# Kernel optimization log

Hardware: AMD Instinct MI355X
Metric: run time of the kernel (lower is better)

## Reference

```python
import jax, jax.numpy as jnp
import numpy as np
from itertools import product

# Static geometry (matches init_kwargs)
Z, H, W = 8, 96, 180
WZ, WH, WW = 2, 6, 12
MZ, MH, MW = Z // WZ, H // WH, W // WW   # 4, 16, 15
WP = WZ * WH * WW                        # 144 tokens per window
WN = MZ * MH * MW                        # 960 windows
DIM, HEADS = 384, 12
DH = DIM // HEADS
SHIFT = (WZ // 2, WH // 2, WW // 2)      # (1, 3, 6)
NBIAS = WZ * WZ * WH * WH * (2 * WW - 1) # 3312 bias entries
WT = MZ * MH                             # 64 window types (vary with Z,H only)


def _position_index():
    zi = np.arange(WZ); zj = -np.arange(WZ) * WZ
    hi = np.arange(WH); hj = -np.arange(WH) * WH
    w = np.arange(WW)
    c1 = np.stack(np.meshgrid(zi, hi, w, indexing='ij')).reshape(3, WP, 1)
    c2 = np.stack(np.meshgrid(zj, hj, w, indexing='ij')).reshape(3, 1, WP)
    coords = (c1 - c2).transpose(1, 2, 0).astype(np.int64)  # (WP, WP, 3)
    coords[:, :, 2] += WW - 1
    coords[:, :, 1] *= 2 * WW - 1
    coords[:, :, 0] *= (2 * WW - 1) * WH * WH
    return coords.sum(-1).reshape(-1)  # (WP*WP,)


def _attention_mask():
    # in_shape divisible by window -> pad mask is all-zero; only shifted-window
    # (non-adjacency) mask remains, exactly as in the torch buffer.
    img = np.ones((Z, H, W), np.float32)
    zs = (slice(0, -WZ), slice(-WZ, -SHIFT[0]), slice(-SHIFT[0], None))
    hs = (slice(0, -WH), slice(-WH, -SHIFT[1]), slice(-SHIFT[1], None))
    ws = (slice(0, -WW), slice(-WW, -SHIFT[2]), slice(-SHIFT[2], None))
    cnt = 0
    for z, h, w in product(zs, hs, ws):
        img[z, h, w] = cnt
        cnt += 1
    mw = img.reshape(MZ, WZ, MH, WH, MW, WW).transpose(0, 2, 4, 1, 3, 5).reshape(WN, WP)
    diff = mw[:, None, :] - mw[:, :, None]
    return np.where(diff != 0, -100.0, 0.0).astype(np.float32)


POS_IDX = jnp.asarray(_position_index())
ATTN_MASK = jnp.asarray(_attention_mask())  # (WN, WP, WP)


def _layernorm(x, w, b, eps=1e-5):
    m = jnp.mean(x, axis=-1, keepdims=True)
    v = jnp.mean(jnp.square(x - m), axis=-1, keepdims=True)
    return (x - m) * jax.lax.rsqrt(v + eps) * w + b


def setup_inputs() -> dict:
    key = jax.random.key(0)
    ks = jax.random.split(key, 8)
    s = 0.02
    return {
        'x': jax.random.normal(ks[0], (1, Z * H * W, DIM), jnp.float32),
        'w_qkv': jax.random.normal(ks[1], (DIM, 3 * DIM), jnp.float32) * s,
        'w_proj': jax.random.normal(ks[2], (DIM, DIM), jnp.float32) * s,
        'b_proj': jnp.zeros((DIM,), jnp.float32),
        'bias_table': jax.random.normal(ks[3], (NBIAS, WT, HEADS), jnp.float32) * 0.02,
        'ln1_w': jnp.ones((DIM,), jnp.float32),
        'ln1_b': jnp.zeros((DIM,), jnp.float32),
        'ln2_w': jnp.ones((DIM,), jnp.float32),
        'ln2_b': jnp.zeros((DIM,), jnp.float32),
        'w1': jax.random.normal(ks[4], (DIM, 4 * DIM), jnp.float32) * s,
        'b1': jnp.zeros((4 * DIM,), jnp.float32),
        'w2': jax.random.normal(ks[5], (4 * DIM, DIM), jnp.float32) * s,
        'b2': jnp.zeros((DIM,), jnp.float32),
    }


def reference(x, w_qkv, w_proj, b_proj, bias_table, ln1_w, ln1_b, ln2_w, ln2_b, w1, b1, w2, b2):
    B = x.shape[0]
    shortcut = x
    # (B, Z*H*W, D) -> (B, Z, H, W, D); pad is identity (divisible shapes)
    xg = x.reshape(B, Z, H, W, DIM)
    xg = jnp.roll(xg, (-SHIFT[0], -SHIFT[1], -SHIFT[2]), axis=(1, 2, 3))
    # window partition -> (B*WN, WP, D) with window order (B, mZ, mH, mW)
    xw = xg.reshape(B, MZ, WZ, MH, WH, MW, WW, DIM)
    xw = xw.transpose(0, 1, 3, 5, 2, 4, 6, 7).reshape(B * WN, WP, DIM)

    # ---- EarthAttention3D ----
    qkv = (xw @ w_qkv).reshape(B * WN, WP, 3, HEADS, DH).transpose(2, 0, 3, 1, 4)
    q = qkv[0] * (DH ** -0.5)
    k, v = qkv[1], qkv[2]
    attn = jnp.einsum('bhid,bhjd->bhij', q, k)  # (B*WN, HEADS, WP, WP)

    # earth-specific bias: one bias per (mZ, mH) window type, shared over B, mW
    bias = bias_table[POS_IDX].reshape(WP, WP, WT, HEADS).transpose(2, 3, 0, 1)
    bias = bias.reshape(MZ, MH, HEADS, WP, WP)
    attn = attn.reshape(B, MZ, MH, MW, HEADS, WP, WP) + bias[None, :, :, None]

    # shifted-window mask
    attn = attn.reshape(B, WN, HEADS, WP, WP) + ATTN_MASK[None, :, None]
    attn = jax.nn.softmax(attn, axis=-1).reshape(B * WN, HEADS, WP, WP)

    out = jnp.einsum('bhij,bhjd->bhid', attn, v)
    out = out.transpose(0, 2, 1, 3).reshape(B * WN, WP, DIM)
    out = out @ w_proj + b_proj

    # ---- window reverse, unroll, crop (identity) ----
    xg = out.reshape(B, MZ, MH, MW, WZ, WH, WW, DIM)
    xg = xg.transpose(0, 1, 4, 2, 5, 3, 6, 7).reshape(B, Z, H, W, DIM)
    xg = jnp.roll(xg, SHIFT, axis=(1, 2, 3))
    attn_out = xg.reshape(B, Z * H * W, DIM)

    # Pangu post-norm residuals (drop_path prob = 0 -> identity)
    x = shortcut + _layernorm(attn_out, ln1_w, ln1_b)
    h = jax.nn.gelu(x @ w1 + b1, approximate=False) @ w2 + b2
    x = x + _layernorm(h, ln2_w, ln2_b)
    return x
```

## Files before the change

### kernel.cpp

```cpp
#include <hip/hip_runtime.h>
#include <hip/hip_bf16.h>
#include <math.h>

typedef __hip_bfloat16 bf16;
typedef __attribute__((ext_vector_type(4))) float f32x4;
typedef __attribute__((ext_vector_type(16))) float f32x16;
typedef __attribute__((ext_vector_type(8))) short s16x8;
typedef __attribute__((ext_vector_type(4))) short s16x4;

#define DEVI __device__ __forceinline__

constexpr int ZD = 8, HD = 96, WD = 180;
constexpr int WZ = 2, WH = 6, WWn = 12;
constexpr int MZ = 4, MH = 16, MW = 15;
constexpr int WP = 144, WN = 960;
constexpr int DIM = 384, HEADS = 12, DH = 32;
constexpr int TOK = ZD * HD * WD;
constexpr size_t TOKDIM = (size_t)TOK * DIM;
constexpr int NC = 3, CM = TOK / NC;

DEVI short f2b(float f) {
    bf16 h = __float2bfloat16(f);
    return *reinterpret_cast<short*>(&h);
}

DEVI int row_to_token(int r) {
    int wn = r / WP;
    int p  = r - wn * WP;
    int mz = wn / (MH * MW);
    int rem = wn - mz * (MH * MW);
    int mh = rem / MW;
    int mw = rem - mh * MW;
    int lz = p / (WH * WWn);
    int rp = p - lz * (WH * WWn);
    int lh = rp / WWn;
    int lw = rp - lh * WWn;
    int zp = mz * WZ + lz + 1;  if (zp >= ZD) zp -= ZD;
    int hp = mh * WH + lh + 3;  if (hp >= HD) hp -= HD;
    int wp = mw * WWn + lw + 6; if (wp >= WD) wp -= WD;
    return (zp * HD + hp) * WD + wp;
}


__global__ __launch_bounds__(256)
void k_fill(float* __restrict__ out, int n, float v) {
    int i = blockIdx.x * blockDim.x + threadIdx.x;
    if (i < n) out[i] = v;
}

__global__ __launch_bounds__(256)
void k_wcast(const float* __restrict__ w, bf16* __restrict__ wt, int K, int N) {
    int idx = blockIdx.x * blockDim.x + threadIdx.x;
    if (idx >= K * N) return;
    int n = idx / K;
    int k = idx - n * K;
    wt[idx] = __float2bfloat16(w[(size_t)k * N + n]);
}

__global__ __launch_bounds__(256)
void k_btr(const float* __restrict__ bt, float* __restrict__ btr) {
    int idx = blockIdx.x * blockDim.x + threadIdx.x;
    if (idx >= 64 * 12 * 3312) return;
    int wth = idx / 3312;
    int pos = idx - wth * 3312;
    btr[idx] = bt[(size_t)pos * 768 + wth] * 1.4426950408889634f;
}

__global__ __launch_bounds__(256)
void k_mktab(const float* __restrict__ btr, bf16* __restrict__ tab) {
    int idx = blockIdx.x * blockDim.x + threadIdx.x;
    if (idx >= 768 * WP * WP) return;
    int t = idx / (WP * WP);
    int e = idx - t * (WP * WP);
    int i = e / WP, j = e - i * WP;
    int wt = t / 12;
    int mz = wt >> 4, mh = wt & 15;
    int lzi = i / 72, ri_ = i - lzi * 72, lhi = ri_ / 12, lwi = ri_ - lhi * 12;
    int lzj = j / 72, rj_ = j - lzj * 72, lhj = rj_ / 12, lwj = rj_ - lhj * 12;
    int cA = lzi * 828 + lhi * 23 + lwi;
    int cB = lzj * 1656 + lhj * 138 + (11 - lwj);
    float vv = btr[(size_t)t * 3312 + cA + cB];
    int zri = (mz == 3) ? (lzi + 1) : 0, zrj = (mz == 3) ? (lzj + 1) : 0;
    int hri = (mh == 15) ? (lhi < 3 ? 1 : 2) : 0, hrj = (mh == 15) ? (lhj < 3 ? 1 : 2) : 0;
    if (zri != zrj || hri != hrj) vv -= 144.26950408889634f;
    tab[idx] = __float2bfloat16(vv);
}

__global__ __launch_bounds__(256)
void k_gather_x(const float* __restrict__ x, bf16* __restrict__ xw) {
    int idx = blockIdx.x * blockDim.x + threadIdx.x;
    if (idx >= TOK * 96) return;
    int r  = idx / 96;
    int c4 = (idx - r * 96) * 4;
    int t  = row_to_token(r);
    const float4 vv = *(const float4*)(x + (size_t)t * DIM + c4);
    s16x4 o;
    o[0] = f2b(vv.x); o[1] = f2b(vv.y); o[2] = f2b(vv.z); o[3] = f2b(vv.w);
    *(s16x4*)((short*)xw + (size_t)r * DIM + c4) = o;
}


DEVI void gload16(const bf16* g, bf16* l) {
    __builtin_amdgcn_global_load_lds(
        (const __attribute__((address_space(1))) void*)g,
        (__attribute__((address_space(3))) void*)l, 16, 0, 0);
}

template <int EPI>
__global__ __launch_bounds__(256)
void k_gemm(const bf16* __restrict__ A, const bf16* __restrict__ BT,
            const float* __restrict__ bias, bf16* __restrict__ out,
            int M, int N, int K) {
    constexpr int BK = 64;
    __shared__ bf16 As[128 * BK];
    __shared__ bf16 Bs[128 * BK];

    const int nb = N >> 7;
    const int g = blockIdx.x;
    const int xcd = g & 7;
    const int ii = g >> 3;
    const int tt = ii / nb;
    const int bm = tt * 8 + xcd;
    const int bn = ii - tt * nb;

    const int tid = threadIdx.x;
    const int lane = tid & 63;
    const int wv = tid >> 6;
    const int wr = wv >> 1;
    const int wc = wv & 1;
    const int l31 = lane & 31, hi = lane >> 5;

    const bf16* Ab = A + (size_t)bm * 128 * K;
    const bf16* Bb = BT + (size_t)bn * 128 * K;

    f32x16 acc[2][2] = {{{}, {}}, {{}, {}}};

    const int kiters = K / BK;
    const int srow = lane >> 3;
    const int scol = ((lane & 7) ^ srow) * 8;

    int ra[2], rb[2], rax[2], rbx[2];
#pragma unroll
    for (int i2 = 0; i2 < 2; i2++) {
        ra[i2] = 64 * wr + 32 * i2 + l31; rax[i2] = ra[i2] & 7;
        rb[i2] = 64 * wc + 32 * i2 + l31; rbx[i2] = rb[i2] & 7;
    }

    for (int kt = 0; kt < kiters; kt++) {
        const int k0 = kt * BK;
#pragma unroll
        for (int i = 0; i < 4; i++) {
            int ch = wv * 4 + i;
            int row = ch * 8 + srow;
            gload16(Ab + (size_t)row * K + k0 + scol, &As[ch * 512]);
            gload16(Bb + (size_t)row * K + k0 + scol, &Bs[ch * 512]);
        }
        asm volatile("s_waitcnt vmcnt(0)" ::: "memory");
        __syncthreads();
#pragma unroll
        for (int kk = 0; kk < 4; kk++) {
            const int s0 = 2 * kk + hi;
            s16x8 af[2], bfv[2];
#pragma unroll
            for (int ni = 0; ni < 2; ni++)
                af[ni] = *(const s16x8*)&Bs[ra[ni] * BK + ((s0 ^ rax[ni]) * 8)];
#pragma unroll
            for (int mi = 0; mi < 2; mi++)
                bfv[mi] = *(const s16x8*)&As[rb[mi] * BK + ((s0 ^ rbx[mi]) * 8)];
#pragma unroll
            for (int ni = 0; ni < 2; ni++)
#pragma unroll
                for (int mi = 0; mi < 2; mi++)
                    acc[ni][mi] = __builtin_amdgcn_mfma_f32_32x32x16_bf16(
                        af[ni], bfv[mi], acc[ni][mi], 0, 0, 0);
        }
        __syncthreads();
    }

    const int tokbase = bm * 128 + 64 * wc + l31;
    const int featbase = bn * 128 + 64 * wr + 4 * hi;
#pragma unroll
    for (int ni = 0; ni < 2; ni++) {
#pragma unroll
        for (int mi = 0; mi < 2; mi++) {
            const int tok = tokbase + 32 * mi;
#pragma unroll
            for (int rq = 0; rq < 4; rq++) {
                const int f0 = featbase + 32 * ni + 8 * rq;
                float v0 = acc[ni][mi][4 * rq + 0];
                float v1 = acc[ni][mi][4 * rq + 1];
                float v2 = acc[ni][mi][4 * rq + 2];
                float v3 = acc[ni][mi][4 * rq + 3];
                if constexpr (EPI == 0) {
                    const int which = f0 / DIM;
                    const int rem = f0 - which * DIM;
                    const int head = rem >> 5, dh = rem & 31;
                    if (which == 0) {
                        v0 *= 0.25503527f; v1 *= 0.25503527f;
                        v2 *= 0.25503527f; v3 *= 0.25503527f;
                    }
                    const int wn = tok / WP, p = tok - wn * WP;
                    s16x4 o; o[0] = f2b(v0); o[1] = f2b(v1); o[2] = f2b(v2); o[3] = f2b(v3);
                    *(s16x4*)(out + (size_t)which * TOKDIM +
                              ((size_t)(wn * HEADS + head) * WP + p) * DH + dh) = o;
                } else if constexpr (EPI == 1) {
                    const float4 bv = *(const float4*)(bias + f0);
                    s16x4 o;
                    o[0] = f2b(v0 + bv.x); o[1] = f2b(v1 + bv.y);
                    o[2] = f2b(v2 + bv.z); o[3] = f2b(v3 + bv.w);
                    *(s16x4*)(out + (size_t)tok * N + f0) = o;
                } else {
                    const float4 bv = *(const float4*)(bias + f0);
                    float g0 = v0 + bv.x, g1 = v1 + bv.y, g2 = v2 + bv.z, g3 = v3 + bv.w;
                    g0 = 0.5f * g0 * (1.0f + erff(g0 * 0.70710678118654752f));
                    g1 = 0.5f * g1 * (1.0f + erff(g1 * 0.70710678118654752f));
                    g2 = 0.5f * g2 * (1.0f + erff(g2 * 0.70710678118654752f));
                    g3 = 0.5f * g3 * (1.0f + erff(g3 * 0.70710678118654752f));
                    s16x4 o; o[0] = f2b(g0); o[1] = f2b(g1); o[2] = f2b(g2); o[3] = f2b(g3);
                    *(s16x4*)(out + (size_t)tok * N + f0) = o;
                }
            }
        }
    }
}

__global__ __launch_bounds__(192)
void k_attn(const bf16* __restrict__ q, const bf16* __restrict__ kmat,
            const bf16* __restrict__ v, const bf16* __restrict__ tab,
            bf16* __restrict__ out) {
    __shared__ bf16 Ks[WP * DH];
    __shared__ bf16 VTs[DH * 168];
    __shared__ bf16 Ps[3][16][168];
    __shared__ unsigned char regn[WP];

    const int bid = blockIdx.x;
    const int wn = bid / HEADS, head = bid - wn * HEADS;
    const int mz = wn / (MH * MW);
    const int rem = wn - mz * (MH * MW);
    const int mh = rem / MW, mw = rem - (rem / MW) * MW;
    const int tile = (mz * MH + mh) * HEADS + head;

    const int tid = threadIdx.x;
    const int lane = tid & 63;
    const int s = tid >> 6;
    const int lg = lane >> 4, lc = lane & 15;

    const size_t base = (size_t)(wn * HEADS + head) * (WP * DH);
    {
        short* vt = (short*)VTs;
#pragma unroll
        for (int e2 = 0; e2 < 3; e2++) {
            int idx = tid + 192 * e2;
            *(s16x8*)(Ks + idx * 8) = *(const s16x8*)(kmat + base + idx * 8);
            s16x8 vv = *(const s16x8*)(v + base + idx * 8);
            int p = idx >> 2;
            int d0 = (idx & 3) * 8;
#pragma unroll
            for (int e = 0; e < 8; e++) vt[(d0 + e) * 168 + p] = vv[e];
        }
        { int d = tid / 6, rm = tid - d * 6;
          *(s16x4*)(vt + d * 168 + 144 + rm * 4) = (s16x4){0, 0, 0, 0}; }
        { short* pz = (short*)&Ps[s][0][0];
          *(s16x4*)(pz + (lane >> 2) * 168 + 144 + (lane & 3) * 4) = (s16x4){0, 0, 0, 0}; }
        if (tid < WP) {
            int lz = tid / 72, rp = tid - lz * 72;
            int lh = rp / 12, lw = rp - lh * 12;
            int zr = (mz == 3) ? (lz + 1) : 0;
            int hr = (mh == 15) ? (lh < 3 ? 1 : 2) : 0;
            int wbit = (lw < 6) ? 1 : 2;
            regn[tid] = (unsigned char)((zr * 3 + hr) * 4 + wbit);
        }
    }
    __syncthreads();

    const f32x4 zf = {0.f, 0.f, 0.f, 0.f};
    const bf16* tb = tab + (size_t)tile * (WP * WP);
    bf16* ob = out + (size_t)wn * (WP * DIM) + head * DH;
    short* ps = (short*)&Ps[s][0][0];
    const bf16* psb = &Ps[s][0][0];

    for (int t = 0; t < 3; t++) {
        const int strip = 3 * s + t;
        const int ib = 16 * strip + 4 * lg;
        s16x8 aq = *(const s16x8*)(q + base + (size_t)(16 * strip + lc) * DH + 8 * lg);
        f32x4 sacc[9];
#pragma unroll
        for (int jt = 0; jt < 9; jt++) {
            s16x8 bk = *(const s16x8*)(Ks + (16 * jt + lc) * DH + 8 * lg);
            sacc[jt] = __builtin_amdgcn_mfma_f32_16x16x32_bf16(aq, bk, zf, 0, 0, 0);
        }
#pragma unroll
        for (int jt = 0; jt < 9; jt++) {
            int j = 16 * jt + lc;
#pragma unroll
            for (int r2 = 0; r2 < 4; r2++)
                sacc[jt][r2] += __bfloat162float(tb[(ib + r2) * WP + j]);
        }
        if (mw == 14) {
            int ri[4];
#pragma unroll
            for (int r2 = 0; r2 < 4; r2++) ri[r2] = regn[ib + r2];
#pragma unroll
            for (int jt = 0; jt < 9; jt++) {
                int rj = regn[16 * jt + lc];
#pragma unroll
                for (int r2 = 0; r2 < 4; r2++) {
                    bool m = ((ri[r2] >> 2) == (rj >> 2)) && ((ri[r2] & 3) != (rj & 3));
                    if (m) sacc[jt][r2] -= 144.2695f;
                }
            }
        }
        float inv[4];
#pragma unroll
        for (int r2 = 0; r2 < 4; r2++) {
            float sum = 0.f;
#pragma unroll
            for (int jt = 0; jt < 9; jt++) {
                float pe = exp2f(sacc[jt][r2]);
                sacc[jt][r2] = pe;
                sum += pe;
            }
#pragma unroll
            for (int o = 1; o < 16; o <<= 1) sum += __shfl_xor(sum, o);
            inv[r2] = 1.0f / sum;
        }
#pragma unroll
        for (int jt = 0; jt < 9; jt++)
#pragma unroll
            for (int r2 = 0; r2 < 4; r2++)
                ps[(4 * lg + r2) * 168 + 16 * jt + lc] = f2b(sacc[jt][r2]);
        f32x4 oacc[2] = {zf, zf};
#pragma unroll
        for (int c = 0; c < 5; c++) {
            s16x8 ap = *(const s16x8*)(psb + lc * 168 + 32 * c + 8 * lg);
#pragma unroll
            for (int nt = 0; nt < 2; nt++) {
                s16x8 bv = *(const s16x8*)(VTs + (16 * nt + lc) * 168 + 32 * c + 8 * lg);
                oacc[nt] = __builtin_amdgcn_mfma_f32_16x16x32_bf16(ap, bv, oacc[nt], 0, 0, 0);
            }
        }
#pragma unroll
        for (int nt = 0; nt < 2; nt++)
#pragma unroll
            for (int r2 = 0; r2 < 4; r2++)
                ob[(size_t)(ib + r2) * DIM + 16 * nt + lc] =
                    __float2bfloat16(oacc[nt][r2] * inv[r2]);
    }
}


__global__ __launch_bounds__(128)
void k_ln1(const bf16* __restrict__ y, const float* __restrict__ x,
           const float* __restrict__ w, const float* __restrict__ b,
           bf16* __restrict__ x1b, int r0) {
    __shared__ float red[4];
    const int rl = blockIdx.x, tid = threadIdx.x;
    const int t = row_to_token(r0 + rl);
    float v[3];
#pragma unroll
    for (int e = 0; e < 3; e++) v[e] = __bfloat162float(y[(size_t)rl * DIM + tid + 128 * e]);
    float s = v[0] + v[1] + v[2];
    float s2 = v[0] * v[0] + v[1] * v[1] + v[2] * v[2];
#pragma unroll
    for (int o = 1; o < 64; o <<= 1) { s += __shfl_xor(s, o); s2 += __shfl_xor(s2, o); }
    const int wv = tid >> 6;
    if ((tid & 63) == 0) { red[wv * 2] = s; red[wv * 2 + 1] = s2; }
    __syncthreads();
    s = red[0] + red[2]; s2 = red[1] + red[3];
    float mean = s * (1.f / 384.f);
    float var = fmaxf(s2 * (1.f / 384.f) - mean * mean, 0.f);
    float rs = rsqrtf(var + 1e-5f);
#pragma unroll
    for (int e = 0; e < 3; e++) {
        int c = tid + 128 * e;
        float o = (v[e] - mean) * rs * w[c] + b[c];
        float xo = x[(size_t)t * DIM + c] + o;
        ((short*)x1b)[(size_t)t * DIM + c] = f2b(xo);
    }
}

__global__ __launch_bounds__(128)
void k_ln2(const bf16* __restrict__ h, const bf16* __restrict__ x1b,
           const float* __restrict__ w, const float* __restrict__ b,
           float* __restrict__ out) {
    __shared__ float red[4];
    const int r = blockIdx.x, tid = threadIdx.x;
    float v[3];
#pragma unroll
    for (int e = 0; e < 3; e++) v[e] = __bfloat162float(h[(size_t)r * DIM + tid + 128 * e]);
    float s = v[0] + v[1] + v[2];
    float s2 = v[0] * v[0] + v[1] * v[1] + v[2] * v[2];
#pragma unroll
    for (int o = 1; o < 64; o <<= 1) { s += __shfl_xor(s, o); s2 += __shfl_xor(s2, o); }
    const int wv = tid >> 6;
    if ((tid & 63) == 0) { red[wv * 2] = s; red[wv * 2 + 1] = s2; }
    __syncthreads();
    s = red[0] + red[2]; s2 = red[1] + red[3];
    float mean = s * (1.f / 384.f);
    float var = fmaxf(s2 * (1.f / 384.f) - mean * mean, 0.f);
    float rs = rsqrtf(var + 1e-5f);
#pragma unroll
    for (int e = 0; e < 3; e++) {
        int c = tid + 128 * e;
        float o = (v[e] - mean) * rs * w[c] + b[c];
        out[(size_t)r * DIM + c] = __bfloat162float(x1b[(size_t)r * DIM + c]) + o;
    }
}


extern "C" void kernel_launch(void* const* d_in, const int* in_sizes, int n_in,
                              void* d_out, int out_size, void* d_ws, size_t ws_size,
                              hipStream_t stream) {
    const float* x      = (const float*)d_in[0];
    const float* w_qkv  = (const float*)d_in[1];
    const float* w_proj = (const float*)d_in[2];
    const float* b_proj = (const float*)d_in[3];
    const float* btab   = (const float*)d_in[4];
    const float* ln1w   = (const float*)d_in[5];
    const float* ln1b   = (const float*)d_in[6];
    const float* ln2w   = (const float*)d_in[7];
    const float* ln2b   = (const float*)d_in[8];
    const float* w1     = (const float*)d_in[9];
    const float* b1     = (const float*)d_in[10];
    const float* w2     = (const float*)d_in[11];
    const float* b2     = (const float*)d_in[12];

    const size_t NEED = 470237184ULL;
    if (ws_size < NEED) {
        k_fill<<<(out_size + 255) / 256, 256, 0, stream>>>((float*)d_out, out_size, 12345.0f);
        return;
    }

    char* ws = (char*)d_ws;
    bf16* wqkvT  = (bf16*)(ws + 0);
    bf16* wprojT = (bf16*)(ws + 884736);
    bf16* w1T    = (bf16*)(ws + 1179648);
    bf16* w2T    = (bf16*)(ws + 2359296);
    float* btr   = (float*)(ws + 3538944);
    bf16* tab    = (bf16*)(ws + 13713408);

    const size_t D1 = 45563904;
    const size_t D2 = 364068864;

    bf16* qkv  = (bf16*)(ws + D1);
    bf16* x1b  = (bf16*)(ws + D1);
    bf16* ytmp = (bf16*)(ws + D1 + 106168320);
    bf16* h1c  = (bf16*)(ws + D1 + 106168320);
    bf16* xw   = (bf16*)(ws + D2);
    bf16* aout = (bf16*)(ws + D2);
    bf16* htmp = (bf16*)(ws + D2);

    k_wcast<<<(442368 + 255) / 256, 256, 0, stream>>>(w_qkv, wqkvT, 384, 1152);
    k_wcast<<<(147456 + 255) / 256, 256, 0, stream>>>(w_proj, wprojT, 384, 384);
    k_wcast<<<(589824 + 255) / 256, 256, 0, stream>>>(w1, w1T, 384, 1536);
    k_wcast<<<(589824 + 255) / 256, 256, 0, stream>>>(w2, w2T, 1536, 384);
    k_btr<<<(2543616 + 255) / 256, 256, 0, stream>>>(btab, btr);
    k_mktab<<<(768 * WP * WP + 255) / 256, 256, 0, stream>>>(btr, tab);
    k_gather_x<<<(TOK * 96 + 255) / 256, 256, 0, stream>>>(x, xw);

    k_gemm<0><<<dim3((TOK / 128) * 9), 256, 0, stream>>>(xw, wqkvT, nullptr, qkv, TOK, 1152, 384);

    k_attn<<<dim3(WN * HEADS), 192, 0, stream>>>(qkv, qkv + TOKDIM, qkv + 2 * TOKDIM, tab, aout);

    for (int c = 0; c < NC; c++) {
        k_gemm<1><<<dim3((CM / 128) * 3), 256, 0, stream>>>(
            aout + (size_t)c * CM * DIM, wprojT, b_proj, ytmp, CM, 384, 384);
        k_ln1<<<dim3(CM), 128, 0, stream>>>(ytmp, x, ln1w, ln1b, x1b, c * CM);
    }

    for (int c = 0; c < NC; c++) {
        k_gemm<2><<<dim3((CM / 128) * 12), 256, 0, stream>>>(
            x1b + (size_t)c * CM * DIM, w1T, b1, h1c, CM, 1536, 384);
        k_gemm<1><<<dim3((CM / 128) * 3), 256, 0, stream>>>(
            h1c, w2T, b2, htmp + (size_t)c * CM * DIM, CM, 384, 1536);
    }

    k_ln2<<<dim3(TOK), 128, 0, stream>>>(htmp, x1b, ln2w, ln2b, (float*)d_out);
}
```

Measured before the change: 1.428 ms.

## Double-buffer GEMM LDS tiles, read K from global in attention, warp-per-row layernorms

The GEMM switches from single-buffered BK=64 tiles to double-buffered BK=32 tiles, so the global-to-LDS load of the next tile overlaps the MFMA work on the current one. The attention kernel stops staging K in shared memory, reads K fragments straight from global memory, and shrinks the padded row stride. Both layernorm kernels now handle one row per wavefront with vectorized bf16 loads, which removes the shared-memory reduction and block barrier. The halved K tile means twice as many barriers per GEMM, and direct global K reads may cost more latency.

```diff
diff --git a/kernel.cpp b/kernel.cpp
--- a/kernel.cpp
+++ b/kernel.cpp
@@ -111,9 +111,9 @@
 void k_gemm(const bf16* __restrict__ A, const bf16* __restrict__ BT,
             const float* __restrict__ bias, bf16* __restrict__ out,
             int M, int N, int K) {
-    constexpr int BK = 64;
-    __shared__ bf16 As[128 * BK];
-    __shared__ bf16 Bs[128 * BK];
+    constexpr int BK = 32;
+    __shared__ bf16 As[2][128 * BK];
+    __shared__ bf16 Bs[2][128 * BK];
 
     const int nb = N >> 7;
     const int g = blockIdx.x;
@@ -133,40 +133,47 @@
     const bf16* Ab = A + (size_t)bm * 128 * K;
     const bf16* Bb = BT + (size_t)bn * 128 * K;
 
+    const int srow = lane >> 2;
+    const int sslot = lane & 3;
+
     f32x16 acc[2][2] = {{{}, {}}, {{}, {}}};
 
+    int ra[2], rb[2], rax[2], rbx[2];
+#pragma unroll
+    for (int i2 = 0; i2 < 2; i2++) {
+        ra[i2] = 64 * wr + 32 * i2 + l31; rax[i2] = ra[i2] & 3;
+        rb[i2] = 64 * wc + 32 * i2 + l31; rbx[i2] = rb[i2] & 3;
+    }
+
     const int kiters = K / BK;
-    const int srow = lane >> 3;
-    const int scol = ((lane & 7) ^ srow) * 8;
-
-    int ra[2], rb[2], rax[2], rbx[2];
-#pragma unroll
-    for (int i2 = 0; i2 < 2; i2++) {
-        ra[i2] = 64 * wr + 32 * i2 + l31; rax[i2] = ra[i2] & 7;
-        rb[i2] = 64 * wc + 32 * i2 + l31; rbx[i2] = rb[i2] & 7;
-    }
-
+
+    auto stage = [&](int buf, int k0) {
+#pragma unroll
+        for (int i = 0; i < 2; i++) {
+            int r = i * 64 + wv * 16 + srow;
+            int sl = (sslot ^ (r & 3)) * 8;
+            gload16(Ab + (size_t)r * K + k0 + sl, &As[buf][i * 2048 + wv * 512]);
+            gload16(Bb + (size_t)r * K + k0 + sl, &Bs[buf][i * 2048 + wv * 512]);
+        }
+    };
+
+    stage(0, 0);
+    asm volatile("s_waitcnt vmcnt(0)" ::: "memory");
+    __syncthreads();
+
+    int cur = 0;
     for (int kt = 0; kt < kiters; kt++) {
-        const int k0 = kt * BK;
-#pragma unroll
-        for (int i = 0; i < 4; i++) {
-            int ch = wv * 4 + i;
-            int row = ch * 8 + srow;
-            gload16(Ab + (size_t)row * K + k0 + scol, &As[ch * 512]);
-            gload16(Bb + (size_t)row * K + k0 + scol, &Bs[ch * 512]);
-        }
-        asm volatile("s_waitcnt vmcnt(0)" ::: "memory");
-        __syncthreads();
-#pragma unroll
-        for (int kk = 0; kk < 4; kk++) {
+        if (kt + 1 < kiters) stage(cur ^ 1, (kt + 1) * BK);
+#pragma unroll
+        for (int kk = 0; kk < 2; kk++) {
             const int s0 = 2 * kk + hi;
             s16x8 af[2], bfv[2];
 #pragma unroll
             for (int ni = 0; ni < 2; ni++)
-                af[ni] = *(const s16x8*)&Bs[ra[ni] * BK + ((s0 ^ rax[ni]) * 8)];
+                af[ni] = *(const s16x8*)&Bs[cur][ra[ni] * BK + ((s0 ^ rax[ni]) * 8)];
 #pragma unroll
             for (int mi = 0; mi < 2; mi++)
-                bfv[mi] = *(const s16x8*)&As[rb[mi] * BK + ((s0 ^ rbx[mi]) * 8)];
+                bfv[mi] = *(const s16x8*)&As[cur][rb[mi] * BK + ((s0 ^ rbx[mi]) * 8)];
 #pragma unroll
             for (int ni = 0; ni < 2; ni++)
 #pragma unroll
@@ -174,7 +181,9 @@
                     acc[ni][mi] = __builtin_amdgcn_mfma_f32_32x32x16_bf16(
                         af[ni], bfv[mi], acc[ni][mi], 0, 0, 0);
         }
+        asm volatile("s_waitcnt vmcnt(0)" ::: "memory");
         __syncthreads();
+        cur ^= 1;
     }
 
     const int tokbase = bm * 128 + 64 * wc + l31;
@@ -228,9 +237,8 @@
 void k_attn(const bf16* __restrict__ q, const bf16* __restrict__ kmat,
             const bf16* __restrict__ v, const bf16* __restrict__ tab,
             bf16* __restrict__ out) {
-    __shared__ bf16 Ks[WP * DH];
-    __shared__ bf16 VTs[DH * 168];
-    __shared__ bf16 Ps[3][16][168];
+    __shared__ bf16 VTs[DH * 164];
+    __shared__ bf16 Ps[3][16 * 164];
     __shared__ unsigned char regn[WP];
 
     const int bid = blockIdx.x;
@@ -251,17 +259,18 @@
 #pragma unroll
         for (int e2 = 0; e2 < 3; e2++) {
             int idx = tid + 192 * e2;
-            *(s16x8*)(Ks + idx * 8) = *(const s16x8*)(kmat + base + idx * 8);
             s16x8 vv = *(const s16x8*)(v + base + idx * 8);
             int p = idx >> 2;
             int d0 = (idx & 3) * 8;
 #pragma unroll
-            for (int e = 0; e < 8; e++) vt[(d0 + e) * 168 + p] = vv[e];
-        }
-        { int d = tid / 6, rm = tid - d * 6;
-          *(s16x4*)(vt + d * 168 + 144 + rm * 4) = (s16x4){0, 0, 0, 0}; }
-        { short* pz = (short*)&Ps[s][0][0];
-          *(s16x4*)(pz + (lane >> 2) * 168 + 144 + (lane & 3) * 4) = (s16x4){0, 0, 0, 0}; }
+            for (int e = 0; e < 8; e++) vt[(d0 + e) * 164 + p] = vv[e];
+        }
+        if (tid < 160) {
+            int d = tid / 5, gq = tid - d * 5;
+            *(s16x4*)(vt + d * 164 + 144 + gq * 4) = (s16x4){0, 0, 0, 0};
+        }
+        { short* pz = (short*)&Ps[s][0];
+          *(s16x4*)(pz + (lane >> 2) * 164 + 144 + (lane & 3) * 4) = (s16x4){0, 0, 0, 0}; }
         if (tid < WP) {
             int lz = tid / 72, rp = tid - lz * 72;
             int lh = rp / 12, lw = rp - lh * 12;
@@ -275,9 +284,10 @@
 
     const f32x4 zf = {0.f, 0.f, 0.f, 0.f};
     const bf16* tb = tab + (size_t)tile * (WP * WP);
+    const bf16* kb = kmat + base;
     bf16* ob = out + (size_t)wn * (WP * DIM) + head * DH;
-    short* ps = (short*)&Ps[s][0][0];
-    const bf16* psb = &Ps[s][0][0];
+    short* ps = (short*)&Ps[s][0];
+    const bf16* psb = &Ps[s][0];
 
     for (int t = 0; t < 3; t++) {
         const int strip = 3 * s + t;
@@ -286,7 +296,7 @@
         f32x4 sacc[9];
 #pragma unroll
         for (int jt = 0; jt < 9; jt++) {
-            s16x8 bk = *(const s16x8*)(Ks + (16 * jt + lc) * DH + 8 * lg);
+            s16x8 bk = *(const s16x8*)(kb + (size_t)(16 * jt + lc) * DH + 8 * lg);
             sacc[jt] = __builtin_amdgcn_mfma_f32_16x16x32_bf16(aq, bk, zf, 0, 0, 0);
         }
 #pragma unroll
@@ -328,14 +338,14 @@
         for (int jt = 0; jt < 9; jt++)
 #pragma unroll
             for (int r2 = 0; r2 < 4; r2++)
-                ps[(4 * lg + r2) * 168 + 16 * jt + lc] = f2b(sacc[jt][r2]);
+                ps[(4 * lg + r2) * 164 + 16 * jt + lc] = f2b(sacc[jt][r2]);
         f32x4 oacc[2] = {zf, zf};
 #pragma unroll
         for (int c = 0; c < 5; c++) {
-            s16x8 ap = *(const s16x8*)(psb + lc * 168 + 32 * c + 8 * lg);
+            s16x8 ap = *(const s16x8*)(psb + lc * 164 + 32 * c + 8 * lg);
 #pragma unroll
             for (int nt = 0; nt < 2; nt++) {
-                s16x8 bv = *(const s16x8*)(VTs + (16 * nt + lc) * 168 + 32 * c + 8 * lg);
+                s16x8 bv = *(const s16x8*)(VTs + (16 * nt + lc) * 164 + 32 * c + 8 * lg);
                 oacc[nt] = __builtin_amdgcn_mfma_f32_16x16x32_bf16(ap, bv, oacc[nt], 0, 0, 0);
             }
         }
@@ -349,61 +359,80 @@
 }
 
 
-__global__ __launch_bounds__(128)
+__global__ __launch_bounds__(256)
 void k_ln1(const bf16* __restrict__ y, const float* __restrict__ x,
            const float* __restrict__ w, const float* __restrict__ b,
            bf16* __restrict__ x1b, int r0) {
-    __shared__ float red[4];
-    const int rl = blockIdx.x, tid = threadIdx.x;
-    const int t = row_to_token(r0 + rl);
-    float v[3];
-#pragma unroll
-    for (int e = 0; e < 3; e++) v[e] = __bfloat162float(y[(size_t)rl * DIM + tid + 128 * e]);
-    float s = v[0] + v[1] + v[2];
-    float s2 = v[0] * v[0] + v[1] * v[1] + v[2] * v[2];
-#pragma unroll
-    for (int o = 1; o < 64; o <<= 1) { s += __shfl_xor(s, o); s2 += __shfl_xor(s2, o); }
-    const int wv = tid >> 6;
-    if ((tid & 63) == 0) { red[wv * 2] = s; red[wv * 2 + 1] = s2; }
-    __syncthreads();
-    s = red[0] + red[2]; s2 = red[1] + red[3];
-    float mean = s * (1.f / 384.f);
+    const int row = blockIdx.x * 4 + (threadIdx.x >> 6);
+    const int l = threadIdx.x & 63;
+    const int t = row_to_token(r0 + row);
+    const short* yr = (const short*)y + (size_t)row * DIM;
+    float v[6];
+#pragma unroll
+    for (int e = 0; e < 3; e++) {
+        int c = 128 * e + 2 * l;
+        unsigned int u = *(const unsigned int*)(yr + c);
+        unsigned int lo = (u & 0xffffu) << 16, hiu = u & 0xffff0000u;
+        v[2 * e]     = *reinterpret_cast<float*>(&lo);
+        v[2 * e + 1] = *reinterpret_cast<float*>(&hiu);
+    }
+    float sum = 0.f, s2 = 0.f;
+#pragma unroll
+    for (int e = 0; e < 6; e++) { sum += v[e]; s2 += v[e] * v[e]; }
+#pragma unroll
+    for (int o = 1; o < 64; o <<= 1) { sum += __shfl_xor(sum, o); s2 += __shfl_xor(s2, o); }
+    float mean = sum * (1.f / 384.f);
     float var = fmaxf(s2 * (1.f / 384.f) - mean * mean, 0.f);
     float rs = rsqrtf(var + 1e-5f);
 #pragma unroll
     for (int e = 0; e < 3; e++) {
-        int c = tid + 128 * e;
-        float o = (v[e] - mean) * rs * w[c] + b[c];
-        float xo = x[(size_t)t * DIM + c] + o;
-        ((short*)x1b)[(size_t)t * DIM + c] = f2b(xo);
-    }
-}
-
-__global__ __launch_bounds__(128)
+        int c = 128 * e + 2 * l;
+        const float2 wv2 = *(const float2*)(w + c);
+        const float2 bv2 = *(const float2*)(b + c);
+        const float2 xx = *(const float2*)(x + (size_t)t * DIM + c);
+        float o0 = (v[2 * e] - mean) * rs * wv2.x + bv2.x + xx.x;
+        float o1 = (v[2 * e + 1] - mean) * rs * wv2.y + bv2.y + xx.y;
+        short2 st; st.x = f2b(o0); st.y = f2b(o1);
+        *(short2*)((short*)x1b + (size_t)t * DIM + c) = st;
+    }
+}
+
+__global__ __launch_bounds__(256)
 void k_ln2(const bf16* __restrict__ h, const bf16* __restrict__ x1b,
            const float* __restrict__ w, const float* __restrict__ b,
            float* __restrict__ out) {
-    __shared__ float red[4];
-    const int r = blockIdx.x, tid = threadIdx.x;
-    float v[3];
-#pragma unroll
-    for (int e = 0; e < 3; e++) v[e] = __bfloat162float(h[(size_t)r * DIM + tid + 128 * e]);
-    float s = v[0] + v[1] + v[2];
-    float s2 = v[0] * v[0] + v[1] * v[1] + v[2] * v[2];
-#pragma unroll
-    for (int o = 1; o < 64; o <<= 1) { s += __shfl_xor(s, o); s2 += __shfl_xor(s2, o); }
-    const int wv = tid >> 6;
-    if ((tid & 63) == 0) { red[wv * 2] = s; red[wv * 2 + 1] = s2; }
-    __syncthreads();
-    s = red[0] + red[2]; s2 = red[1] + red[3];
-    float mean = s * (1.f / 384.f);
+    const int row = blockIdx.x * 4 + (threadIdx.x >> 6);
+    const int l = threadIdx.x & 63;
+    const short* hr = (const short*)h + (size_t)row * DIM;
+    float v[6];
+#pragma unroll
+    for (int e = 0; e < 3; e++) {
+        int c = 128 * e + 2 * l;
+        unsigned int u = *(const unsigned int*)(hr + c);
+        unsigned int lo = (u & 0xffffu) << 16, hiu = u & 0xffff0000u;
+        v[2 * e]     = *reinterpret_cast<float*>(&lo);
+        v[2 * e + 1] = *reinterpret_cast<float*>(&hiu);
+    }
+    float sum = 0.f, s2 = 0.f;
+#pragma unroll
+    for (int e = 0; e < 6; e++) { sum += v[e]; s2 += v[e] * v[e]; }
+#pragma unroll
+    for (int o = 1; o < 64; o <<= 1) { sum += __shfl_xor(sum, o); s2 += __shfl_xor(s2, o); }
+    float mean = sum * (1.f / 384.f);
     float var = fmaxf(s2 * (1.f / 384.f) - mean * mean, 0.f);
     float rs = rsqrtf(var + 1e-5f);
+    const short* xr = (const short*)x1b + (size_t)row * DIM;
 #pragma unroll
     for (int e = 0; e < 3; e++) {
-        int c = tid + 128 * e;
-        float o = (v[e] - mean) * rs * w[c] + b[c];
-        out[(size_t)r * DIM + c] = __bfloat162float(x1b[(size_t)r * DIM + c]) + o;
+        int c = 128 * e + 2 * l;
+        const float2 wv2 = *(const float2*)(w + c);
+        const float2 bv2 = *(const float2*)(b + c);
+        unsigned int u = *(const unsigned int*)(xr + c);
+        unsigned int lo = (u & 0xffffu) << 16, hiu = u & 0xffff0000u;
+        float2 o2;
+        o2.x = (v[2 * e] - mean) * rs * wv2.x + bv2.x + *reinterpret_cast<float*>(&lo);
+        o2.y = (v[2 * e + 1] - mean) * rs * wv2.y + bv2.y + *reinterpret_cast<float*>(&hiu);
+        *(float2*)(out + (size_t)row * DIM + c) = o2;
     }
 }
 
@@ -465,7 +494,7 @@
     for (int c = 0; c < NC; c++) {
         k_gemm<1><<<dim3((CM / 128) * 3), 256, 0, stream>>>(
             aout + (size_t)c * CM * DIM, wprojT, b_proj, ytmp, CM, 384, 384);
-        k_ln1<<<dim3(CM), 128, 0, stream>>>(ytmp, x, ln1w, ln1b, x1b, c * CM);
+        k_ln1<<<dim3(CM / 4), 256, 0, stream>>>(ytmp, x, ln1w, ln1b, x1b, c * CM);
     }
 
     for (int c = 0; c < NC; c++) {
@@ -475,5 +504,5 @@
             h1c, w2T, b2, htmp + (size_t)c * CM * DIM, CM, 384, 1536);
     }
 
-    k_ln2<<<dim3(TOK), 128, 0, stream>>>(htmp, x1b, ln2w, ln2b, (float*)d_out);
-}
+    k_ln2<<<dim3(TOK / 4), 256, 0, stream>>>(htmp, x1b, ln2w, ln2b, (float*)d_out);
+}
```

Measured after the change: 1.549 ms. 8.5% more time.
